# Performance work log

Measured on AMD Instinct MI355X. Metric: run time of the kernel, lower is better.

Reference implementation:

```python
import jax, jax.numpy as jnp
import numpy as np

N_NODES = 100000
N_EDGES = 800000
IN_FEATS = 128
HIDDEN = 64
SCALE = 0.5 ** 0.5  # sqrt(0.5) residual scale
BN_EPS = 1e-5


def setup_inputs() -> dict:
    key = jax.random.key(0)
    ks = jax.random.split(key, 12)
    return {
        "src": jax.random.randint(ks[0], (N_EDGES,), 0, N_NODES, dtype=jnp.int64)
        if jax.config.jax_enable_x64 else jax.random.randint(ks[0], (N_EDGES,), 0, N_NODES),
        "dst": jax.random.randint(ks[1], (N_EDGES,), 0, N_NODES),
        "x": jax.random.normal(ks[2], (N_NODES, IN_FEATS), dtype=jnp.float32),
        "fc_w": jax.random.normal(ks[3], (IN_FEATS, HIDDEN), dtype=jnp.float32) * 0.05,
        "fc_b": jax.random.normal(ks[4], (HIDDEN,), dtype=jnp.float32) * 0.05,
        "w1": jax.random.normal(ks[5], (HIDDEN, HIDDEN), dtype=jnp.float32) * 0.05,
        "b1": jax.random.normal(ks[6], (HIDDEN,), dtype=jnp.float32) * 0.05,
        "w2": jax.random.normal(ks[7], (HIDDEN, HIDDEN), dtype=jnp.float32) * 0.05,
        "b2": jax.random.normal(ks[8], (HIDDEN,), dtype=jnp.float32) * 0.05,
        "gamma": jax.random.normal(ks[9], (HIDDEN,), dtype=jnp.float32) * 0.05 + 1.0,
        "beta": jax.random.normal(ks[10], (HIDDEN,), dtype=jnp.float32) * 0.05,
    }


def _graph_conv(h, w, b, src, dst, norm_src, norm_dst, n_nodes):
    # DGL GraphConv, norm='both': y = D_in^{-1/2} A D_out^{-1/2} (h W) + b
    h = h @ w                                   # [N, H]
    m = h[src] * norm_src[:, None]              # gather + src-degree norm, [E, H]
    agg = jax.ops.segment_sum(m, dst, num_segments=n_nodes)  # scatter-add, [N, H]
    return agg * norm_dst[:, None] + b


def reference(src, dst, x, fc_w, fc_b, w1, b1, w2, b2, gamma, beta):
    n_nodes = x.shape[0]
    ones_e = jnp.ones(src.shape[0], dtype=x.dtype)
    deg_out = jnp.clip(jax.ops.segment_sum(ones_e, src, num_segments=n_nodes), 1.0)
    deg_in = jnp.clip(jax.ops.segment_sum(ones_e, dst, num_segments=n_nodes), 1.0)
    norm_src = (deg_out ** -0.5)[src]           # per-edge source normalization
    norm_dst = deg_in ** -0.5                   # per-node destination normalization

    h = x @ fc_w + fc_b                          # fc: [N, H]
    h = (h + _graph_conv(h, w1, b1, src, dst, norm_src, norm_dst, n_nodes)) * SCALE
    h = (h + _graph_conv(h, w2, b2, src, dst, norm_src, norm_dst, n_nodes)) * SCALE

    # BatchNorm1d (training-mode batch statistics over nodes, biased variance)
    mu = h.mean(axis=0)
    var = ((h - mu) ** 2).mean(axis=0)
    h = (h - mu) * jax.lax.rsqrt(var + BN_EPS) * gamma + beta
    return h
```

## Files before the change

kernel.cpp:

```cpp
#include <hip/hip_runtime.h>

#define HIDDEN 64
#define INFEAT 128
#define SCALE_C 0.70710678118654752f
#define BN_EPS 1e-5f
#define AGG_GRID 2048
#define RED_BLK 32

__device__ __forceinline__ float rlf(float v, int l){
  return __int_as_float(__builtin_amdgcn_readlane(__float_as_int(v), l));
}

template<int KDIM, bool ADDB, bool FUSET>
__device__ __forceinline__ void gemm_body(int bid, const float* __restrict__ X,
    const float* __restrict__ W, const float* __restrict__ B,
    float* __restrict__ Y, const float* __restrict__ W2, float* __restrict__ T, int N)
{
  __shared__ float smem[64 * 65];
  const int tid  = threadIdx.x;
  const int lane = tid & 63;
  const int wid  = __builtin_amdgcn_readfirstlane(tid >> 6);
  const int c0 = wid * 16;
  const int base = bid * 64;
  const int gnode = base + lane;

  float acc[16];
  #pragma unroll
  for (int c = 0; c < 16; ++c) acc[c] = ADDB ? B[c0 + c] : 0.f;

  constexpr int NCHUNK = KDIM / 32;
  #pragma unroll 1
  for (int ck = 0; ck < NCHUNK; ++ck){
    __syncthreads();
    #pragma unroll
    for (int i = 0; i < 2; ++i){
      int f  = i * 256 + tid;
      int nd = f >> 3;
      int kq = f & 7;
      float4 v = make_float4(0.f, 0.f, 0.f, 0.f);
      if (base + nd < N)
        v = *(const float4*)(X + (size_t)(base + nd) * KDIM + ck * 32 + kq * 4);
      float* p = &smem[nd * 65 + kq * 4];
      p[0] = v.x; p[1] = v.y; p[2] = v.z; p[3] = v.w;
    }
    __syncthreads();
    const float* wrow = W + (size_t)ck * 32 * HIDDEN + c0;
    #pragma unroll
    for (int k = 0; k < 32; ++k){
      float xv = smem[lane * 65 + k];
      #pragma unroll
      for (int c = 0; c < 16; ++c)
        acc[c] = fmaf(xv, wrow[k * HIDDEN + c], acc[c]);
    }
  }

  if (gnode < N){
    float4* yp = (float4*)(Y + (size_t)gnode * HIDDEN + c0);
    #pragma unroll
    for (int j = 0; j < 4; ++j)
      yp[j] = make_float4(acc[4*j], acc[4*j+1], acc[4*j+2], acc[4*j+3]);
  }

  if constexpr (FUSET){
    __syncthreads();
    #pragma unroll
    for (int c = 0; c < 16; ++c) smem[lane * 65 + c0 + c] = acc[c];
    __syncthreads();
    float tacc[16];
    #pragma unroll
    for (int c = 0; c < 16; ++c) tacc[c] = 0.f;
    const float* w2r = W2 + c0;
    #pragma unroll
    for (int k = 0; k < 64; ++k){
      float hv = smem[lane * 65 + k];
      #pragma unroll
      for (int c = 0; c < 16; ++c)
        tacc[c] = fmaf(hv, w2r[k * HIDDEN + c], tacc[c]);
    }
    if (gnode < N){
      float4* tp = (float4*)(T + (size_t)gnode * HIDDEN + c0);
      #pragma unroll
      for (int j = 0; j < 4; ++j)
        tp[j] = make_float4(tacc[4*j], tacc[4*j+1], tacc[4*j+2], tacc[4*j+3]);
    }
  }
}

__device__ __forceinline__ int role_gemm_idx(int b, int GB, int TOT, int& histIdx){
  int fb  = (int)(((long)b * GB) / TOT);
  int fb1 = (int)(((long)(b + 1) * GB) / TOT);
  histIdx = b - fb;
  return (fb1 > fb) ? fb : -1;
}

__global__ __launch_bounds__(256) void k_mega1(const int* __restrict__ dst,
    int* __restrict__ degI, int E,
    const float* __restrict__ x, const float* __restrict__ fc_w,
    const float* __restrict__ fc_b, float* __restrict__ h,
    const float* __restrict__ w1, float* __restrict__ t, int N, int GB, int TOT){
  int hIdx;
  int g = role_gemm_idx(blockIdx.x, GB, TOT, hIdx);
  if (g >= 0) gemm_body<INFEAT, true, true>(g, x, fc_w, fc_b, h, w1, t, N);
  else {
    int e0 = hIdx * 2048 + threadIdx.x;
    #pragma unroll
    for (int i = 0; i < 8; ++i){
      int e = e0 + i * 256;
      if (e < E) atomicAdd(&degI[dst[e]], 1);
    }
  }
}

__global__ __launch_bounds__(256) void k_place(const int* __restrict__ src,
    const int* __restrict__ dst, int* __restrict__ cursor,
    int* __restrict__ cs, int* __restrict__ degO, int E){
  int e0 = blockIdx.x * 2048 + threadIdx.x;
  #pragma unroll
  for (int i = 0; i < 8; ++i){
    int e = e0 + i * 256;
    if (e < E){
      int s = src[e];
      int pos = atomicAdd(&cursor[dst[e]], 1);
      cs[pos] = s;
      atomicAdd(&degO[s], 1);
    }
  }
}

__global__ void k_scan1(const int* __restrict__ deg, int* __restrict__ bsum, int N){
  __shared__ int sh[256];
  int t = threadIdx.x;
  int i = blockIdx.x * 256 + t;
  sh[t] = (i < N) ? deg[i] : 0;
  __syncthreads();
  for (int ofs = 128; ofs > 0; ofs >>= 1){
    if (t < ofs) sh[t] += sh[t + ofs];
    __syncthreads();
  }
  if (t == 0) bsum[blockIdx.x] = sh[0];
}

__global__ void k_scan2(int* __restrict__ bsum, int NB){
  __shared__ int sh[512];
  int t = threadIdx.x;
  int v = (t < NB) ? bsum[t] : 0;
  sh[t] = v;
  __syncthreads();
  for (int ofs = 1; ofs < 512; ofs <<= 1){
    int u = (t >= ofs) ? sh[t - ofs] : 0;
    __syncthreads();
    sh[t] += u;
    __syncthreads();
  }
  if (t < NB) bsum[t] = sh[t] - v;
}

__global__ void k_scan3(const int* __restrict__ degI, const int* __restrict__ bofs,
                        int* __restrict__ rp, int* __restrict__ cursor,
                        float* __restrict__ norm_in, int N, int E){
  __shared__ int sh[256];
  int t = threadIdx.x;
  int i = blockIdx.x * 256 + t;
  int v = (i < N) ? degI[i] : 0;
  sh[t] = v;
  __syncthreads();
  for (int ofs = 1; ofs < 256; ofs <<= 1){
    int u = (t >= ofs) ? sh[t - ofs] : 0;
    __syncthreads();
    sh[t] += u;
    __syncthreads();
  }
  if (i < N){
    int excl = sh[t] - v + bofs[blockIdx.x];
    rp[i] = excl;
    cursor[i] = excl;
    if (i == N - 1) rp[N] = E;
    norm_in[i] = rsqrtf((float)max(v, 1));
  }
}

template<bool PRE>
__device__ __forceinline__ float4 gather_pre4(const int* __restrict__ cs,
    const float* __restrict__ t, const int* __restrict__ degO,
    int start, int end, int g, int s4, int i0, int i1, int i2, int i3)
{
  float4 acc = make_float4(0.f, 0.f, 0.f, 0.f);
  int j0 = start + g;
  if (j0 >= end) return acc;
  {
    const bool b1 = (j0 + 4 < end);
    const float4 r0 = *(const float4*)(t + (size_t)i0 * HIDDEN + s4);
    const float4 r1 = *(const float4*)(t + (size_t)i1 * HIDDEN + s4);
    const float w0 = PRE ? 1.f : rsqrtf((float)degO[i0]);
    const float w1 = b1 ? (PRE ? 1.f : rsqrtf((float)degO[i1])) : 0.f;
    acc.x = fmaf(r0.x, w0, acc.x); acc.y = fmaf(r0.y, w0, acc.y);
    acc.z = fmaf(r0.z, w0, acc.z); acc.w = fmaf(r0.w, w0, acc.w);
    acc.x = fmaf(r1.x, w1, acc.x); acc.y = fmaf(r1.y, w1, acc.y);
    acc.z = fmaf(r1.z, w1, acc.z); acc.w = fmaf(r1.w, w1, acc.w);
    j0 += 8;
  }
  if (j0 >= end) return acc;
  {
    const bool b1 = (j0 + 4 < end);
    const float4 r0 = *(const float4*)(t + (size_t)i2 * HIDDEN + s4);
    const float4 r1 = *(const float4*)(t + (size_t)i3 * HIDDEN + s4);
    const float w0 = PRE ? 1.f : rsqrtf((float)degO[i2]);
    const float w1 = b1 ? (PRE ? 1.f : rsqrtf((float)degO[i3])) : 0.f;
    acc.x = fmaf(r0.x, w0, acc.x); acc.y = fmaf(r0.y, w0, acc.y);
    acc.z = fmaf(r0.z, w0, acc.z); acc.w = fmaf(r0.w, w0, acc.w);
    acc.x = fmaf(r1.x, w1, acc.x); acc.y = fmaf(r1.y, w1, acc.y);
    acc.z = fmaf(r1.z, w1, acc.z); acc.w = fmaf(r1.w, w1, acc.w);
    j0 += 8;
  }
  while (j0 < end){
    int a0 = cs[j0];
    int a1 = (j0 + 4 < end) ? cs[j0 + 4] : a0;
    const bool b1 = (j0 + 4 < end);
    const float4 r0 = *(const float4*)(t + (size_t)a0 * HIDDEN + s4);
    const float4 r1 = *(const float4*)(t + (size_t)a1 * HIDDEN + s4);
    const float w0 = PRE ? 1.f : rsqrtf((float)degO[a0]);
    const float w1 = b1 ? (PRE ? 1.f : rsqrtf((float)degO[a1])) : 0.f;
    acc.x = fmaf(r0.x, w0, acc.x); acc.y = fmaf(r0.y, w0, acc.y);
    acc.z = fmaf(r0.z, w0, acc.z); acc.w = fmaf(r0.w, w0, acc.w);
    acc.x = fmaf(r1.x, w1, acc.x); acc.y = fmaf(r1.y, w1, acc.y);
    acc.z = fmaf(r1.z, w1, acc.z); acc.w = fmaf(r1.w, w1, acc.w);
    j0 += 8;
  }
  return acc;
}

__device__ __forceinline__ void pf4(const int* __restrict__ cs, int s, int e, int g,
                                    int& p0, int& p1, int& p2, int& p3){
  p0 = (s + g      < e) ? cs[s + g]      : 0;
  p1 = (s + g + 4  < e) ? cs[s + g + 4]  : 0;
  p2 = (s + g + 8  < e) ? cs[s + g + 8]  : 0;
  p3 = (s + g + 12 < e) ? cs[s + g + 12] : 0;
}

__device__ __forceinline__ float4 xreduce4(float4 a){
  #pragma unroll
  for (int m = 16; m <= 32; m <<= 1){
    a.x += __shfl_xor(a.x, m, 64);
    a.y += __shfl_xor(a.y, m, 64);
    a.z += __shfl_xor(a.z, m, 64);
    a.w += __shfl_xor(a.w, m, 64);
  }
  return a;
}

template<bool BN, bool PRE, bool FUSET2>
__global__ __launch_bounds__(256, 4) void k_agg(const int* __restrict__ rp, const int* __restrict__ cs,
    const float* __restrict__ t, const int* __restrict__ degO,
    const float* __restrict__ norm_in, const float* __restrict__ b,
    const float* __restrict__ w2, float* __restrict__ h,
    float* __restrict__ t2, float* __restrict__ bnpart, int N)
{
  const int tid  = threadIdx.x;
  const int lane = tid & 63;
  const int g    = lane >> 4;
  const int s    = lane & 15;
  const int s4   = s * 4;
  const int wv = (blockIdx.x * 256 + tid) >> 6;
  const int nw = (gridDim.x * 256) >> 6;
  const float4 bv = ((const float4*)b)[s];
  float4 s1 = make_float4(0.f,0.f,0.f,0.f), s2v = make_float4(0.f,0.f,0.f,0.f);

  float w2c[64];
  if constexpr (FUSET2){
    #pragma unroll
    for (int k = 0; k < 64; ++k) w2c[k] = w2[k * HIDDEN + lane];
  }

  int nA = wv;
  int sA = 0, eA = 0, pA0 = 0, pA1 = 0, pA2 = 0, pA3 = 0; float niA = 0.f;
  float4 hA = make_float4(0.f,0.f,0.f,0.f);
  if (nA < N){
    sA = rp[nA]; eA = rp[nA + 1];
    niA = norm_in[nA];
    hA = *(const float4*)(h + (size_t)nA * HIDDEN + s4);
    pf4(cs, sA, eA, g, pA0, pA1, pA2, pA3);
  }
  int nB = nA + nw;
  int sB = 0, eB = 0;
  if (nB < N){ sB = rp[nB]; eB = rp[nB + 1]; }

  for (int n = nA; n < N; n += nw){
    const int nC = n + 2 * nw;
    int sC = 0, eC = 0;
    if (nC < N){ sC = rp[nC]; eC = rp[nC + 1]; }
    int pB0 = 0, pB1 = 0, pB2 = 0, pB3 = 0; float niB = 0.f;
    float4 hB = make_float4(0.f,0.f,0.f,0.f);
    if (n + nw < N){
      pf4(cs, sB, eB, g, pB0, pB1, pB2, pB3);
      niB = norm_in[n + nw];
      hB = *(const float4*)(h + (size_t)(n + nw) * HIDDEN + s4);
    }

    float4 acc = gather_pre4<PRE>(cs, t, degO, sA, eA, g, s4, pA0, pA1, pA2, pA3);
    acc = xreduce4(acc);
    const size_t rowo = (size_t)n * HIDDEN;
    float4 v;
    v.x = (hA.x + acc.x * niA + bv.x) * SCALE_C;
    v.y = (hA.y + acc.y * niA + bv.y) * SCALE_C;
    v.z = (hA.z + acc.z * niA + bv.z) * SCALE_C;
    v.w = (hA.w + acc.w * niA + bv.w) * SCALE_C;
    if (g == 0){
      *(float4*)(h + rowo + s4) = v;
      if (BN){
        s1.x += v.x; s1.y += v.y; s1.z += v.z; s1.w += v.w;
        s2v.x += v.x*v.x; s2v.y += v.y*v.y; s2v.z += v.z*v.z; s2v.w += v.w*v.w;
      }
    }
    if constexpr (FUSET2){
      float nout = rsqrtf((float)max(degO[n], 1));
      float ta0 = 0.f, ta1 = 0.f, ta2 = 0.f, ta3 = 0.f;
      #pragma unroll
      for (int k = 0; k < 64; k += 4){
        const int ln = k >> 2;
        ta0 = fmaf(rlf(v.x, ln), w2c[k],     ta0);
        ta1 = fmaf(rlf(v.y, ln), w2c[k + 1], ta1);
        ta2 = fmaf(rlf(v.z, ln), w2c[k + 2], ta2);
        ta3 = fmaf(rlf(v.w, ln), w2c[k + 3], ta3);
      }
      t2[rowo + lane] = ((ta0 + ta1) + (ta2 + ta3)) * nout;
    }
    sA = sB; eA = eB; pA0 = pB0; pA1 = pB1; pA2 = pB2; pA3 = pB3; niA = niB; hA = hB;
    sB = sC; eB = eC;
  }

  if (BN){
    __shared__ float l1[4][64], l2[4][64];
    const int wid = tid >> 6;
    if (g == 0){
      l1[wid][s4+0] = s1.x; l1[wid][s4+1] = s1.y; l1[wid][s4+2] = s1.z; l1[wid][s4+3] = s1.w;
      l2[wid][s4+0] = s2v.x; l2[wid][s4+1] = s2v.y; l2[wid][s4+2] = s2v.z; l2[wid][s4+3] = s2v.w;
    }
    __syncthreads();
    if (tid < 64){
      float a1 = l1[0][tid] + l1[1][tid] + l1[2][tid] + l1[3][tid];
      float a2 = l2[0][tid] + l2[1][tid] + l2[2][tid] + l2[3][tid];
      bnpart[blockIdx.x * 128 + tid] = a1;
      bnpart[blockIdx.x * 128 + 64 + tid] = a2;
    }
  }
}

__global__ __launch_bounds__(256) void k_bnred(const float* __restrict__ bnpart,
    float* __restrict__ bnred, int nblk){
  int col  = threadIdx.x & 127;
  int half = threadIdx.x >> 7;
  int rows = nblk / RED_BLK;
  int r0 = blockIdx.x * rows;
  float s = 0.f;
  for (int r = half; r < rows; r += 2)
    s += bnpart[(size_t)(r0 + r) * 128 + col];
  __shared__ float sh[256];
  sh[threadIdx.x] = s;
  __syncthreads();
  if (threadIdx.x < 128)
    bnred[blockIdx.x * 128 + threadIdx.x] = sh[threadIdx.x] + sh[threadIdx.x + 128];
}

__global__ void k_bnfin(const float* __restrict__ bnred,
    const float* __restrict__ gamma, const float* __restrict__ beta,
    float* __restrict__ bnab, float invN){
  int c = threadIdx.x;
  float s1 = 0.f, s2 = 0.f;
  #pragma unroll
  for (int b = 0; b < RED_BLK; ++b){ s1 += bnred[b*128 + c]; s2 += bnred[b*128 + 64 + c]; }
  float mu  = s1 * invN;
  float var = s2 * invN - mu * mu;
  float rstd = rsqrtf(var + BN_EPS);
  float sc = gamma[c] * rstd;
  bnab[c] = sc;
  bnab[64 + c] = beta[c] - mu * sc;
}

__global__ void k_bnapply(float* __restrict__ h, const float* __restrict__ bnab, long total4){
  long i = (long)blockIdx.x * blockDim.x + threadIdx.x;
  if (i < total4){
    int c = (int)((i * 4) & 63);
    float4 v = ((float4*)h)[i];
    v.x = fmaf(v.x, bnab[c],     bnab[64 + c]);
    v.y = fmaf(v.y, bnab[c + 1], bnab[65 + c]);
    v.z = fmaf(v.z, bnab[c + 2], bnab[66 + c]);
    v.w = fmaf(v.w, bnab[c + 3], bnab[67 + c]);
    ((float4*)h)[i] = v;
  }
}

extern "C" void kernel_launch(void* const* d_in, const int* in_sizes, int n_in,
                              void* d_out, int out_size, void* d_ws, size_t ws_size,
                              hipStream_t stream){
  const int* src = (const int*)d_in[0];
  const int* dst = (const int*)d_in[1];
  const float* x     = (const float*)d_in[2];
  const float* fc_w  = (const float*)d_in[3];
  const float* fc_b  = (const float*)d_in[4];
  const float* w1    = (const float*)d_in[5];
  const float* b1    = (const float*)d_in[6];
  const float* w2    = (const float*)d_in[7];
  const float* b2    = (const float*)d_in[8];
  const float* gamma = (const float*)d_in[9];
  const float* beta  = (const float*)d_in[10];
  const int E = in_sizes[0];
  const int N = in_sizes[2] / INFEAT;
  const int NB  = (N + 255) / 256;
  const int EB8 = (E + 2047) / 2048;
  const int GB  = (N + 63) / 64;
  const int TOT = EB8 + GB;

  float* h = (float*)d_out;

  const size_t Nh = (size_t)N * HIDDEN;
  float* t        = (float*)d_ws;
  float* t2       = t + Nh;
  float* norm_in  = t2 + Nh;
  float* bnpart   = norm_in + N;
  float* bnred    = bnpart + AGG_GRID * 128;
  float* bnab     = bnred + RED_BLK * 128;
  int*   degO     = (int*)(bnab + 128);
  int*   degI     = degO + N;
  int*   rp       = degI + N;
  int*   cursor   = rp + N + 1;
  int*   bsum     = cursor + N;
  int*   cs       = bsum + 512;

  hipMemsetAsync(degO, 0, 2 * (size_t)N * sizeof(int), stream);

  k_mega1<<<TOT, 256, 0, stream>>>(dst, degI, E,
                                   x, fc_w, fc_b, h, w1, t, N, GB, TOT);

  k_scan1<<<NB, 256, 0, stream>>>(degI, bsum, N);
  k_scan2<<<1, 512, 0, stream>>>(bsum, NB);
  k_scan3<<<NB, 256, 0, stream>>>(degI, bsum, rp, cursor, norm_in, N, E);

  k_place<<<EB8, 256, 0, stream>>>(src, dst, cursor, cs, degO, E);

  k_agg<false, false, true><<<AGG_GRID, 256, 0, stream>>>(
      rp, cs, t, degO, norm_in, b1, w2, h, t2, nullptr, N);
  k_agg<true, true, false><<<AGG_GRID, 256, 0, stream>>>(
      rp, cs, t2, degO, norm_in, b2, nullptr, h, nullptr, bnpart, N);

  k_bnred<<<RED_BLK, 256, 0, stream>>>(bnpart, bnred, AGG_GRID);
  k_bnfin<<<1, 64, 0, stream>>>(bnred, gamma, beta, bnab, 1.0f / (float)N);
  long total4 = (long)N * HIDDEN / 4;
  k_bnapply<<<(int)((total4 + 255) / 256), 256, 0, stream>>>(h, bnab, total4);
}
```

Measured before the change: 363.6 us.

## Record per-edge histogram rank and fuse CSR placement with the first GEMM

The in-degree histogram kernel now stores each edge's atomic return value as its rank within its destination. A placement pass then writes cs[rp[dst]+rank] with no cursor atomics, and that pass is co-scheduled with the fc/W1 GEMM blocks in one mega kernel instead of putting the GEMM alongside the histogram. This removes one set of atomics and the cursor array, and overlaps placement with the compute-bound GEMM. The cost is an extra E-sized rank buffer written and read, and the histogram kernel now runs on its own without GEMM overlap.

Result: faster. 339.2 us (-6.7%).

```diff
diff --git a/kernel.cpp b/kernel.cpp
--- a/kernel.cpp
+++ b/kernel.cpp
@@ -93,36 +93,35 @@
   return (fb1 > fb) ? fb : -1;
 }
 
-__global__ __launch_bounds__(256) void k_mega1(const int* __restrict__ dst,
-    int* __restrict__ degI, int E,
-    const float* __restrict__ x, const float* __restrict__ fc_w,
-    const float* __restrict__ fc_b, float* __restrict__ h,
-    const float* __restrict__ w1, float* __restrict__ t, int N, int GB, int TOT){
-  int hIdx;
-  int g = role_gemm_idx(blockIdx.x, GB, TOT, hIdx);
-  if (g >= 0) gemm_body<INFEAT, true, true>(g, x, fc_w, fc_b, h, w1, t, N);
-  else {
-    int e0 = hIdx * 2048 + threadIdx.x;
-    #pragma unroll
-    for (int i = 0; i < 8; ++i){
-      int e = e0 + i * 256;
-      if (e < E) atomicAdd(&degI[dst[e]], 1);
-    }
-  }
-}
-
-__global__ __launch_bounds__(256) void k_place(const int* __restrict__ src,
-    const int* __restrict__ dst, int* __restrict__ cursor,
-    int* __restrict__ cs, int* __restrict__ degO, int E){
+__global__ __launch_bounds__(256) void k_hist(const int* __restrict__ dst,
+    int* __restrict__ degI, int* __restrict__ rank, int E){
   int e0 = blockIdx.x * 2048 + threadIdx.x;
   #pragma unroll
   for (int i = 0; i < 8; ++i){
     int e = e0 + i * 256;
-    if (e < E){
-      int s = src[e];
-      int pos = atomicAdd(&cursor[dst[e]], 1);
-      cs[pos] = s;
-      atomicAdd(&degO[s], 1);
+    if (e < E) rank[e] = atomicAdd(&degI[dst[e]], 1);
+  }
+}
+
+__global__ __launch_bounds__(256) void k_mega2(const int* __restrict__ src,
+    const int* __restrict__ dst, const int* __restrict__ rank,
+    const int* __restrict__ rp, int* __restrict__ cs, int* __restrict__ degO, int E,
+    const float* __restrict__ x, const float* __restrict__ fc_w,
+    const float* __restrict__ fc_b, float* __restrict__ h,
+    const float* __restrict__ w1, float* __restrict__ t, int N, int GB, int TOT){
+  int pIdx;
+  int g = role_gemm_idx(blockIdx.x, GB, TOT, pIdx);
+  if (g >= 0) gemm_body<INFEAT, true, true>(g, x, fc_w, fc_b, h, w1, t, N);
+  else {
+    int e0 = pIdx * 2048 + threadIdx.x;
+    #pragma unroll
+    for (int i = 0; i < 8; ++i){
+      int e = e0 + i * 256;
+      if (e < E){
+        int s = src[e];
+        cs[rp[dst[e]] + rank[e]] = s;
+        atomicAdd(&degO[s], 1);
+      }
     }
   }
 }
@@ -156,8 +155,7 @@
 }
 
 __global__ void k_scan3(const int* __restrict__ degI, const int* __restrict__ bofs,
-                        int* __restrict__ rp, int* __restrict__ cursor,
-                        float* __restrict__ norm_in, int N, int E){
+                        int* __restrict__ rp, float* __restrict__ norm_in, int N, int E){
   __shared__ int sh[256];
   int t = threadIdx.x;
   int i = blockIdx.x * 256 + t;
@@ -173,7 +171,6 @@
   if (i < N){
     int excl = sh[t] - v + bofs[blockIdx.x];
     rp[i] = excl;
-    cursor[i] = excl;
     if (i == N - 1) rp[N] = E;
     norm_in[i] = rsqrtf((float)max(v, 1));
   }
@@ -422,20 +419,20 @@
   int*   degO     = (int*)(bnab + 128);
   int*   degI     = degO + N;
   int*   rp       = degI + N;
-  int*   cursor   = rp + N + 1;
-  int*   bsum     = cursor + N;
-  int*   cs       = bsum + 512;
+  int*   bsum     = rp + N + 1;
+  int*   rank     = bsum + 512;
+  int*   cs       = rank + E;
 
   hipMemsetAsync(degO, 0, 2 * (size_t)N * sizeof(int), stream);
 
-  k_mega1<<<TOT, 256, 0, stream>>>(dst, degI, E,
-                                   x, fc_w, fc_b, h, w1, t, N, GB, TOT);
+  k_hist<<<EB8, 256, 0, stream>>>(dst, degI, rank, E);
 
   k_scan1<<<NB, 256, 0, stream>>>(degI, bsum, N);
   k_scan2<<<1, 512, 0, stream>>>(bsum, NB);
-  k_scan3<<<NB, 256, 0, stream>>>(degI, bsum, rp, cursor, norm_in, N, E);
-
-  k_place<<<EB8, 256, 0, stream>>>(src, dst, cursor, cs, degO, E);
+  k_scan3<<<NB, 256, 0, stream>>>(degI, bsum, rp, norm_in, N, E);
+
+  k_mega2<<<TOT, 256, 0, stream>>>(src, dst, rank, rp, cs, degO, E,
+                                   x, fc_w, fc_b, h, w1, t, N, GB, TOT);
 
   k_agg<false, false, true><<<AGG_GRID, 256, 0, stream>>>(
       rp, cs, t, degO, norm_in, b1, w2, h, t2, nullptr, N);
```
